# Optimization experiments

Measured on AMD Instinct MI355X. Metric: run time of the kernel, lower is better.

The kernel has to match this reference:

```python
import jax, jax.numpy as jnp
import numpy as np

D_MODEL = 1024
NHEAD = 16
DFF = 4096
EPS = 1e-5


def layer_norm(x, g, b, eps=EPS):
    mu = jnp.mean(x, axis=-1, keepdims=True)
    var = jnp.var(x, axis=-1, keepdims=True)
    return (x - mu) * jax.lax.rsqrt(var + eps) * g + b


def setup_inputs() -> dict:
    key = jax.random.key(0)
    ks = jax.random.split(key, 8)
    S, N, E = 1024, 8, D_MODEL
    s = 0.02
    return {
        "src": jax.random.normal(ks[0], (S, N, E), dtype=jnp.float32),
        "in_proj_w": jax.random.normal(ks[1], (3 * E, E), dtype=jnp.float32) * s,
        "in_proj_b": jnp.zeros((3 * E,), dtype=jnp.float32),
        "out_w": jax.random.normal(ks[2], (E, E), dtype=jnp.float32) * s,
        "out_b": jnp.zeros((E,), dtype=jnp.float32),
        "w1": jax.random.normal(ks[3], (DFF, E), dtype=jnp.float32) * s,
        "b1": jnp.zeros((DFF,), dtype=jnp.float32),
        "w2": jax.random.normal(ks[4], (E, DFF), dtype=jnp.float32) * s,
        "b2": jnp.zeros((E,), dtype=jnp.float32),
        "ln1_g": jnp.ones((E,), dtype=jnp.float32),
        "ln1_b": jnp.zeros((E,), dtype=jnp.float32),
        "ln2_g": jnp.ones((E,), dtype=jnp.float32),
        "ln2_b": jnp.zeros((E,), dtype=jnp.float32),
    }


def reference(src, in_proj_w, in_proj_b, out_w, out_b, w1, b1, w2, b2,
              ln1_g, ln1_b, ln2_g, ln2_b):
    S, N, E = src.shape
    H = NHEAD
    D = E // H
    scale = 1.0 / jnp.sqrt(jnp.asarray(D, src.dtype))

    # fused QKV projection (PyTorch in_proj): [S,N,3E]
    qkv = src @ in_proj_w.T + in_proj_b
    q, k, v = jnp.split(qkv, 3, axis=-1)
    # [S,N,E] -> [N,H,S,D]
    def to_heads(t):
        return t.reshape(S, N, H, D).transpose(1, 2, 0, 3)
    q, k, v = to_heads(q), to_heads(k), to_heads(v)

    # explicit QK^T / softmax / AV (need_weights=True path)
    scores = jnp.einsum('nhsd,nhtd->nhst', q * scale, k)  # [N,H,S,S]
    attn = jax.nn.softmax(scores, axis=-1)
    ctx = jnp.einsum('nhst,nhtd->nhsd', attn, v)          # [N,H,S,D]
    ctx = ctx.transpose(2, 0, 1, 3).reshape(S, N, E)
    attn_out = ctx @ out_w.T + out_b

    # avg over heads (PyTorch default average_attn_weights=True): [N,S,S]
    attn_weights = jnp.mean(attn, axis=1)

    # post-norm residual structure (norm_first=False), dropout=0 (eval)
    x = layer_norm(src + attn_out, ln1_g, ln1_b)
    ff = jax.nn.relu(x @ w1.T + b1) @ w2.T + b2
    x = layer_norm(x + ff, ln2_g, ln2_b)
    return x, attn_weights
```

## Files before the change

kernel.cpp:

```cpp
#include <hip/hip_runtime.h>

typedef __attribute__((ext_vector_type(4))) float f32x4;
typedef __attribute__((ext_vector_type(8))) short short8;
typedef __attribute__((ext_vector_type(4))) unsigned short u16x4;

#define MFMA(a,b,c) __builtin_amdgcn_mfma_f32_16x16x32_bf16(a,b,c,0,0,0)

__device__ __forceinline__ unsigned short f2bf(float x){
    union { float f; unsigned int u; } c; c.f = x;
    unsigned int u = c.u;
    unsigned int r = (u + 0x7fffu + ((u >> 16) & 1u)) >> 16;
    return (unsigned short)r;
}
__device__ __forceinline__ unsigned short tf2bf(float x){
    union { float f; unsigned int u; } c; c.f = x;
    return (unsigned short)(c.u >> 16);
}
__device__ __forceinline__ float bf2f(unsigned short h){
    union { unsigned int u; float f; } c; c.u = ((unsigned int)h) << 16;
    return c.f;
}

__device__ __forceinline__ void load16_lds(const unsigned short* g, unsigned short* l){
    __builtin_amdgcn_global_load_lds(
        (const __attribute__((address_space(1))) unsigned int*)g,
        (__attribute__((address_space(3))) unsigned int*)l, 16, 0, 0);
}

#define SWZ_IDX(row, col, stride) \
    ((row)*(stride) + (((((col) >> 3) ^ ((row) & 7)) << 3) | ((col) & 7)))

__global__ __launch_bounds__(256) void cast_f32_bf16(const float* __restrict__ in,
                                                     unsigned short* __restrict__ out, int n4){
    int i = blockIdx.x * 256 + threadIdx.x;
    if (i < n4){
        const float4* in4 = (const float4*)in;
        float4 v = in4[i];
        u16x4 o;
        o[0] = f2bf(v.x); o[1] = f2bf(v.y); o[2] = f2bf(v.z); o[3] = f2bf(v.w);
        ((u16x4*)out)[i] = o;
    }
}

template<int OUT_BF16, int RELU>
__global__ __launch_bounds__(512) void gemm256(const unsigned short* __restrict__ A,
                                               const unsigned short* __restrict__ W,
                                               const float* __restrict__ bias,
                                               void* __restrict__ Cout,
                                               int M, int N, int K)
{
    __shared__ unsigned short Asw[2][256*64];
    __shared__ unsigned short Bsw[2][256*64];
    const int tid  = threadIdx.x;
    const int wave = tid >> 6, lane = tid & 63;
    const int wr = wave >> 2, wc = wave & 3;
    const int lr = lane & 15, lg = lane >> 4;
    const int bm = blockIdx.x, bn = blockIdx.y;

    f32x4 acc[8][4] = {};

    const unsigned short* Ab = A + (size_t)bm*256*K;
    const unsigned short* Wb = W + (size_t)bn*256*K;

    auto stage = [&](int buf, int k0){
        #pragma unroll
        for (int i = 0; i < 4; ++i){
            int c = i*512 + tid;
            int row = c >> 3, sl = (c & 7) ^ (row & 7);
            load16_lds(Ab + (size_t)row*K + k0 + sl*8, &Asw[buf][0] + (size_t)c*8);
        }
        #pragma unroll
        for (int i = 0; i < 4; ++i){
            int c = i*512 + tid;
            int row = c >> 3, sl = (c & 7) ^ (row & 7);
            load16_lds(Wb + (size_t)row*K + k0 + sl*8, &Bsw[buf][0] + (size_t)c*8);
        }
    };

    stage(0, 0);
    const int NT = K >> 6;
    for (int t = 0; t < NT; ++t){
        const int cur = t & 1;
        if (t + 1 < NT){
            stage(cur ^ 1, (t+1) << 6);
            asm volatile("s_waitcnt vmcnt(8)" ::: "memory");
        } else {
            asm volatile("s_waitcnt vmcnt(0)" ::: "memory");
        }
        __builtin_amdgcn_s_barrier();
        asm volatile("" ::: "memory");
        const unsigned short* Al = &Asw[cur][0];
        const unsigned short* Bl = &Bsw[cur][0];
        #pragma unroll
        for (int kk = 0; kk < 2; ++kk){
            short8 af[8], bf[4];
            #pragma unroll
            for (int mi = 0; mi < 8; ++mi)
                af[mi] = *(const short8*)(Al + SWZ_IDX(wr*128 + mi*16 + lr, kk*32 + lg*8, 64));
            #pragma unroll
            for (int ni = 0; ni < 4; ++ni)
                bf[ni] = *(const short8*)(Bl + SWZ_IDX(wc*64 + ni*16 + lr, kk*32 + lg*8, 64));
            __builtin_amdgcn_s_setprio(1);
            #pragma unroll
            for (int mi = 0; mi < 8; ++mi)
                #pragma unroll
                for (int ni = 0; ni < 4; ++ni)
                    acc[mi][ni] = MFMA(af[mi], bf[ni], acc[mi][ni]);
            __builtin_amdgcn_s_setprio(0);
        }
        asm volatile("" ::: "memory");
        __builtin_amdgcn_s_barrier();
    }

    #pragma unroll
    for (int ni = 0; ni < 4; ++ni){
        int col = bn*256 + wc*64 + ni*16 + lr;
        float bv = bias ? bias[col] : 0.0f;
        #pragma unroll
        for (int mi = 0; mi < 8; ++mi){
            int row0 = bm*256 + wr*128 + mi*16 + lg*4;
            #pragma unroll
            for (int j = 0; j < 4; ++j){
                float v = acc[mi][ni][j] + bv;
                if (RELU) v = v > 0.0f ? v : 0.0f;
                if (OUT_BF16) ((unsigned short*)Cout)[(size_t)(row0+j)*N + col] = f2bf(v);
                else          ((float*)Cout)[(size_t)(row0+j)*N + col] = v;
            }
        }
    }
}

template<int OUT_BF16, int RELU>
__global__ __launch_bounds__(512) void gemm256x128(const unsigned short* __restrict__ A,
                                                   const unsigned short* __restrict__ W,
                                                   const float* __restrict__ bias,
                                                   void* __restrict__ Cout,
                                                   int M, int N, int K)
{
    __shared__ unsigned short Asw[2][256*64];
    __shared__ unsigned short Bsw[2][128*64];
    const int tid  = threadIdx.x;
    const int wave = tid >> 6, lane = tid & 63;
    const int wr = wave >> 1, wc = wave & 1;
    const int lr = lane & 15, lg = lane >> 4;
    const int bm = blockIdx.x, bn = blockIdx.y;

    f32x4 acc[4][4] = {};

    const unsigned short* Ab = A + (size_t)bm*256*K;
    const unsigned short* Wb = W + (size_t)bn*128*K;

    auto stage = [&](int buf, int k0){
        #pragma unroll
        for (int i = 0; i < 4; ++i){
            int c = i*512 + tid;
            int row = c >> 3, sl = (c & 7) ^ (row & 7);
            load16_lds(Ab + (size_t)row*K + k0 + sl*8, &Asw[buf][0] + (size_t)c*8);
        }
        #pragma unroll
        for (int i = 0; i < 2; ++i){
            int c = i*512 + tid;
            int row = c >> 3, sl = (c & 7) ^ (row & 7);
            load16_lds(Wb + (size_t)row*K + k0 + sl*8, &Bsw[buf][0] + (size_t)c*8);
        }
    };

    stage(0, 0);
    const int NT = K >> 6;
    for (int t = 0; t < NT; ++t){
        const int cur = t & 1;
        if (t + 1 < NT){
            stage(cur ^ 1, (t+1) << 6);
            asm volatile("s_waitcnt vmcnt(6)" ::: "memory");
        } else {
            asm volatile("s_waitcnt vmcnt(0)" ::: "memory");
        }
        __builtin_amdgcn_s_barrier();
        asm volatile("" ::: "memory");
        const unsigned short* Al = &Asw[cur][0];
        const unsigned short* Bl = &Bsw[cur][0];
        #pragma unroll
        for (int kk = 0; kk < 2; ++kk){
            short8 af[4], bf[4];
            #pragma unroll
            for (int mi = 0; mi < 4; ++mi)
                af[mi] = *(const short8*)(Al + SWZ_IDX(wr*64 + mi*16 + lr, kk*32 + lg*8, 64));
            #pragma unroll
            for (int ni = 0; ni < 4; ++ni)
                bf[ni] = *(const short8*)(Bl + SWZ_IDX(wc*64 + ni*16 + lr, kk*32 + lg*8, 64));
            __builtin_amdgcn_s_setprio(1);
            #pragma unroll
            for (int mi = 0; mi < 4; ++mi)
                #pragma unroll
                for (int ni = 0; ni < 4; ++ni)
                    acc[mi][ni] = MFMA(af[mi], bf[ni], acc[mi][ni]);
            __builtin_amdgcn_s_setprio(0);
        }
        asm volatile("" ::: "memory");
        __builtin_amdgcn_s_barrier();
    }

    #pragma unroll
    for (int ni = 0; ni < 4; ++ni){
        int col = bn*128 + wc*64 + ni*16 + lr;
        float bv = bias ? bias[col] : 0.0f;
        #pragma unroll
        for (int mi = 0; mi < 4; ++mi){
            int row0 = bm*256 + wr*64 + mi*16 + lg*4;
            #pragma unroll
            for (int j = 0; j < 4; ++j){
                float v = acc[mi][ni][j] + bv;
                if (RELU) v = v > 0.0f ? v : 0.0f;
                if (OUT_BF16) ((unsigned short*)Cout)[(size_t)(row0+j)*N + col] = f2bf(v);
                else          ((float*)Cout)[(size_t)(row0+j)*N + col] = v;
            }
        }
    }
}

__global__ __launch_bounds__(256) void transpose_v(const unsigned short* __restrict__ qkv,
                                                   unsigned short* __restrict__ vt)
{
    __shared__ unsigned short tile[64][80];
    const int tt = blockIdx.x, h = blockIdx.y, n = blockIdx.z;
    const int tid = threadIdx.x;
    #pragma unroll
    for (int i = 0; i < 2; ++i){
        int c = i*256 + tid;
        int row = c >> 3, cc = c & 7;
        short8 v = *(const short8*)(qkv + ((size_t)(tt*64+row)*8 + n)*3072 + 2048 + h*64 + cc*8);
        *(short8*)&tile[row][cc*8] = v;
    }
    __syncthreads();
    #pragma unroll
    for (int i = 0; i < 2; ++i){
        int c = i*256 + tid;
        int drow = c >> 3, cc = c & 7;
        short8 o;
        #pragma unroll
        for (int j = 0; j < 8; ++j) o[j] = tile[cc*8+j][drow];
        *(short8*)(vt + ((size_t)(n*16+h)*64 + drow)*1024 + tt*64 + cc*8) = o;
    }
}

template<int STORE_P8>
__global__ __launch_bounds__(256) void attn_fused(const unsigned short* __restrict__ qkv,
                                                  const unsigned short* __restrict__ vt,
                                                  float* __restrict__ stats,
                                                  unsigned short* __restrict__ ctx,
                                                  unsigned char* __restrict__ p8)
{
    __shared__ unsigned short qs[64*64];
    __shared__ unsigned short kt[2][64*64];
    __shared__ unsigned short vtile[2][64*64];
    __shared__ unsigned short pt[64*64];
    __shared__ float wl[4][64];
    __shared__ float rowinv[64];
    const int qb = blockIdx.x, h = blockIdx.y, n = blockIdx.z;
    const int tid = threadIdx.x;
    const int wave = tid >> 6, lane = tid & 63;
    const int lr = lane & 15, lg = lane >> 4;
    const int s0 = qb * 64;
    const float scale = 0.125f;
    const size_t plane = ((size_t)(n*16 + h)) << 20;

    #pragma unroll
    for (int i = 0; i < 2; ++i){
        int c = i*256 + tid;
        int row = c >> 3, cc = c & 7;
        *(short8*)(qs + SWZ_IDX(row, cc*8, 64)) =
            *(const short8*)(qkv + ((size_t)(s0+row)*8 + n)*3072 + h*64 + cc*8);
    }

    auto stageKV = [&](int buf, int tt){
        #pragma unroll
        for (int i = 0; i < 2; ++i){
            int c = wave*128 + i*64 + lane;
            int row = c >> 3, sl = (c & 7) ^ (row & 7);
            load16_lds(qkv + ((size_t)(tt*64+row)*8 + n)*3072 + 1024 + h*64 + sl*8,
                       &kt[buf][0] + (size_t)c*8);
            load16_lds(vt + ((size_t)(n*16+h)*64 + row)*1024 + tt*64 + sl*8,
                       &vtile[buf][0] + (size_t)c*8);
        }
    };

    stageKV(0, 0);
    __syncthreads();

    float lsum[4][4] = {};
    f32x4 av[4] = {};

    for (int tt = 0; tt < 16; ++tt){
        const int cur = tt & 1;
        if (tt + 1 < 16){
            stageKV(cur ^ 1, tt + 1);
            asm volatile("s_waitcnt vmcnt(4)" ::: "memory");
        } else {
            asm volatile("s_waitcnt vmcnt(0)" ::: "memory");
        }
        asm volatile("" ::: "memory");

        f32x4 acc[4] = {};
        #pragma unroll
        for (int kk = 0; kk < 2; ++kk){
            short8 b = *(const short8*)(&kt[cur][0] + SWZ_IDX(wave*16 + lr, kk*32 + lg*8, 64));
            __builtin_amdgcn_s_setprio(1);
            #pragma unroll
            for (int mi = 0; mi < 4; ++mi){
                short8 a = *(const short8*)(qs + SWZ_IDX(mi*16 + lr, kk*32 + lg*8, 64));
                acc[mi] = MFMA(a, b, acc[mi]);
            }
            __builtin_amdgcn_s_setprio(0);
        }
        unsigned short pv16[4][4];
        #pragma unroll
        for (int mi = 0; mi < 4; ++mi)
            #pragma unroll
            for (int j = 0; j < 4; ++j){
                float p = __expf(fminf(acc[mi][j] * scale, 80.0f));
                lsum[mi][j] += p;
                pv16[mi][j] = tf2bf(p);
            }

        __builtin_amdgcn_s_barrier();
        asm volatile("" ::: "memory");
        #pragma unroll
        for (int mi = 0; mi < 4; ++mi)
            #pragma unroll
            for (int j = 0; j < 4; ++j)
                pt[SWZ_IDX(mi*16 + lg*4 + j, wave*16 + lr, 64)] = pv16[mi][j];
        asm volatile("" ::: "memory");
        __builtin_amdgcn_s_barrier();

        #pragma unroll
        for (int kk = 0; kk < 2; ++kk){
            short8 b = *(const short8*)(&vtile[cur][0] + SWZ_IDX(wave*16 + lr, kk*32 + lg*8, 64));
            __builtin_amdgcn_s_setprio(1);
            #pragma unroll
            for (int mi = 0; mi < 4; ++mi){
                short8 a = *(const short8*)(pt + SWZ_IDX(mi*16 + lr, kk*32 + lg*8, 64));
                av[mi] = MFMA(a, b, av[mi]);
            }
            __builtin_amdgcn_s_setprio(0);
        }

        if (STORE_P8){
            #pragma unroll
            for (int i = 0; i < 2; ++i){
                int c = i*256 + tid;
                int prow = c >> 3, pcc = c & 7;
                short8 pv = *(const short8*)(pt + SWZ_IDX(prow, pcc*8, 64));
                unsigned int w0 = 0, w1 = 0;
                #pragma unroll
                for (int j = 0; j < 4; ++j){
                    unsigned int q = (unsigned int)fminf(bf2f((unsigned short)pv[j])*16.0f + 0.5f, 255.0f);
                    w0 |= q << (8*j);
                }
                #pragma unroll
                for (int j = 4; j < 8; ++j){
                    unsigned int q = (unsigned int)fminf(bf2f((unsigned short)pv[j])*16.0f + 0.5f, 255.0f);
                    w1 |= q << (8*(j-4));
                }
                uint2* dst = (uint2*)(p8 + plane + (size_t)(s0+prow)*1024 + tt*64 + pcc*8);
                *dst = make_uint2(w0, w1);
            }
        }
    }

    #pragma unroll
    for (int mi = 0; mi < 4; ++mi)
        #pragma unroll
        for (int j = 0; j < 4; ++j){
            float v = lsum[mi][j];
            v += __shfl_xor(v, 1);
            v += __shfl_xor(v, 2);
            v += __shfl_xor(v, 4);
            v += __shfl_xor(v, 8);
            if (lr == 0) wl[wave][mi*16 + lg*4 + j] = v;
        }
    __syncthreads();
    if (tid < 64){
        float l = wl[0][tid] + wl[1][tid] + wl[2][tid] + wl[3][tid];
        float inv = 1.0f / l;
        rowinv[tid] = inv;
        stats[((size_t)(n*16+h)*1024) + s0 + tid] = inv * 0.0625f;
    }
    __syncthreads();

    #pragma unroll
    for (int mi = 0; mi < 4; ++mi)
        #pragma unroll
        for (int j = 0; j < 4; ++j){
            int lrow = mi*16 + lg*4 + j;
            int srow = s0 + lrow;
            int d = wave*16 + lr;
            ctx[((size_t)srow*8 + n)*1024 + h*64 + d] = f2bf(av[mi][j] * rowinv[lrow]);
        }
}

__global__ __launch_bounds__(256) void attw_from_p8(const unsigned char* __restrict__ p8,
                                                    const float* __restrict__ stats,
                                                    float* __restrict__ attw)
{
    __shared__ float c[16];
    const int bid = blockIdx.x;
    const int n = bid >> 10, s = bid & 1023;
    const int tid = threadIdx.x;
    if (tid < 16) c[tid] = stats[(((size_t)(n*16 + tid)) << 10) + s] * (1.0f/16.0f);
    __syncthreads();
    float a0=0.f, a1=0.f, a2=0.f, a3=0.f;
    const unsigned char* base = p8 + ((size_t)n << 24) + ((size_t)s << 10) + tid*4;
    #pragma unroll
    for (int h = 0; h < 16; ++h){
        unsigned int v = *(const unsigned int*)(base + ((size_t)h << 20));
        float ch = c[h];
        a0 += (float)( v         & 255u) * ch;
        a1 += (float)((v >> 8 )  & 255u) * ch;
        a2 += (float)((v >> 16)  & 255u) * ch;
        a3 += (float)( v >> 24         ) * ch;
    }
    float4 o; o.x=a0; o.y=a1; o.z=a2; o.w=a3;
    *(float4*)(attw + ((size_t)bid << 10) + tid*4) = o;
}

__global__ __launch_bounds__(256) void attn_mean(const unsigned short* __restrict__ qkv,
                                                 const float* __restrict__ stats,
                                                 float* __restrict__ attw)
{
    __shared__ unsigned short qs[16*1024];
    __shared__ unsigned short kv[2][4][16*128];
    __shared__ float smL[16][16];
    const int qb = blockIdx.x, n = blockIdx.y;
    const int tid = threadIdx.x;
    const int wave = tid >> 6, lane = tid & 63;
    const int lr = lane & 15, lg = lane >> 4;
    const int s0 = qb * 16;
    const float scale = 0.125f;

    {
        int head = tid >> 4, row = tid & 15;
        smL[head][row] = stats[((size_t)(n*16+head)*1024) + s0 + row];
    }
    #pragma unroll
    for (int i = 0; i < 8; ++i){
        int c = i*256 + tid;
        int row = c >> 7, cc = c & 127;
        *(short8*)(qs + SWZ_IDX(row, cc*8, 1024)) =
            *(const short8*)(qkv + ((size_t)(s0+row)*8 + n)*3072 + cc*8);
    }

    unsigned short* kvw = &kv[0][wave][0];
    const int KVBUF = 4*16*128;

    auto stage = [&](int buf, int tt, int g){
        #pragma unroll
        for (int i = 0; i < 4; ++i){
            int c2 = i*64 + lane;
            int rw = c2 >> 4;
            int sd = c2 & 15;
            int sl = sd ^ (rw & 7);
            int trow = tt*64 + wave*16 + rw;
            load16_lds(qkv + ((size_t)trow*8 + n)*3072 + 1024 + g*128 + sl*8,
                       kvw + buf*KVBUF + i*512);
        }
    };

    __syncthreads();
    stage(0, 0, 0);

    float* obase = attw + (size_t)n*1024*1024;
    int r = 0;
    for (int tt = 0; tt < 16; ++tt){
        f32x4 racc = {0.0f, 0.0f, 0.0f, 0.0f};
        for (int g = 0; g < 8; ++g, ++r){
            int nr = r + 1;
            if (nr < 128) stage(nr & 1, nr >> 3, nr & 7);
            if (r < 127) asm volatile("s_waitcnt vmcnt(4)" ::: "memory");
            else         asm volatile("s_waitcnt vmcnt(0)" ::: "memory");
            const unsigned short* kb = kvw + (r & 1)*KVBUF;
            #pragma unroll
            for (int hh = 0; hh < 2; ++hh){
                f32x4 acc = {0.0f, 0.0f, 0.0f, 0.0f};
                #pragma unroll
                for (int kk = 0; kk < 2; ++kk){
                    short8 b = *(const short8*)(kb + SWZ_IDX(lr, hh*64 + kk*32 + lg*8, 128));
                    short8 a = *(const short8*)(qs + SWZ_IDX(lr, g*128 + hh*64 + kk*32 + lg*8, 1024));
                    acc = MFMA(a, b, acc);
                }
                #pragma unroll
                for (int j = 0; j < 4; ++j){
                    float sm = smL[g*2 + hh][lg*4 + j];
                    racc[j] += __expf(fminf(acc[j]*scale, 80.0f)) * sm;
                }
            }
        }
        #pragma unroll
        for (int j = 0; j < 4; ++j)
            obase[(size_t)(s0 + lg*4 + j)*1024 + tt*64 + wave*16 + lr] = racc[j];
    }
}

__global__ __launch_bounds__(256) void add_ln(const float* __restrict__ a,
                                              const float* __restrict__ b,
                                              const float* __restrict__ g,
                                              const float* __restrict__ be,
                                              float* __restrict__ out32,
                                              unsigned short* __restrict__ outbf)
{
    __shared__ float red[8];
    const int row = blockIdx.x;
    const int tid = threadIdx.x;
    const int wave = tid >> 6, lane = tid & 63;
    float4 va = ((const float4*)(a + (size_t)row*1024))[tid];
    float4 vb = ((const float4*)(b + (size_t)row*1024))[tid];
    float x0 = va.x + vb.x, x1 = va.y + vb.y, x2 = va.z + vb.z, x3 = va.w + vb.w;
    float s  = x0 + x1 + x2 + x3;
    float sq = x0*x0 + x1*x1 + x2*x2 + x3*x3;
    #pragma unroll
    for (int off = 1; off < 64; off <<= 1){
        s  += __shfl_xor(s,  off);
        sq += __shfl_xor(sq, off);
    }
    if (lane == 0){ red[wave] = s; red[4+wave] = sq; }
    __syncthreads();
    s  = red[0] + red[1] + red[2] + red[3];
    sq = red[4] + red[5] + red[6] + red[7];
    float mean = s * (1.0f/1024.0f);
    float var  = sq * (1.0f/1024.0f) - mean*mean;
    float rstd = rsqrtf(var + 1e-5f);
    int c = tid * 4;
    float4 vg = ((const float4*)(g  + c))[0];
    float4 vbeta = ((const float4*)(be + c))[0];
    float y0 = (x0-mean)*rstd*vg.x + vbeta.x;
    float y1 = (x1-mean)*rstd*vg.y + vbeta.y;
    float y2 = (x2-mean)*rstd*vg.z + vbeta.z;
    float y3 = (x3-mean)*rstd*vg.w + vbeta.w;
    float4 o; o.x=y0; o.y=y1; o.z=y2; o.w=y3;
    ((float4*)(out32 + (size_t)row*1024))[tid] = o;
    if (outbf){
        u16x4 ob; ob[0]=f2bf(y0); ob[1]=f2bf(y1); ob[2]=f2bf(y2); ob[3]=f2bf(y3);
        ((u16x4*)(outbf + (size_t)row*1024))[tid] = ob;
    }
}

extern "C" void kernel_launch(void* const* d_in, const int* in_sizes, int n_in,
                              void* d_out, int out_size, void* d_ws, size_t ws_size,
                              hipStream_t stream)
{
    (void)in_sizes; (void)n_in; (void)out_size;
    const float* src  = (const float*)d_in[0];
    const float* wqkv = (const float*)d_in[1];
    const float* bqkv = (const float*)d_in[2];
    const float* wout = (const float*)d_in[3];
    const float* bout = (const float*)d_in[4];
    const float* w1   = (const float*)d_in[5];
    const float* b1   = (const float*)d_in[6];
    const float* w2   = (const float*)d_in[7];
    const float* b2   = (const float*)d_in[8];
    const float* g1   = (const float*)d_in[9];
    const float* be1  = (const float*)d_in[10];
    const float* g2   = (const float*)d_in[11];
    const float* be2  = (const float*)d_in[12];

    char* ws = (char*)d_ws;
    const size_t MB = 1ull << 20;
    const bool fastp = (ws_size >= 250*MB);

    unsigned short *wqkv_bf, *wout_bf, *w1_bf, *w2_bf, *src_bf, *x1_bf;
    unsigned short *qkv_bf, *vt_bf, *ff1_bf, *ctx_bf;
    float *attn_out, *ff2_f32, *x1_f32, *stats;
    unsigned char* P8 = nullptr;

    if (fastp){
        wqkv_bf = (unsigned short*)(ws + 0*MB);
        wout_bf = (unsigned short*)(ws + 6*MB);
        w1_bf   = (unsigned short*)(ws + 8*MB);
        w2_bf   = (unsigned short*)(ws + 16*MB);
        src_bf  = (unsigned short*)(ws + 24*MB);
        x1_bf   = (unsigned short*)(ws + 24*MB);
        qkv_bf  = (unsigned short*)(ws + 40*MB);
        vt_bf   = (unsigned short*)(ws + 88*MB);
        ff1_bf  = (unsigned short*)(ws + 40*MB);
        ctx_bf  = (unsigned short*)(ws + 104*MB);
        stats   = (float*)(ws + 120*MB);
        P8      = (unsigned char*)(ws + 121*MB);
        attn_out= (float*)(ws + 121*MB);
        ff2_f32 = (float*)(ws + 121*MB);
        x1_f32  = (float*)(ws + 153*MB);
    } else {
        wqkv_bf = (unsigned short*)(ws + 0*MB);
        wout_bf = (unsigned short*)(ws + 6*MB);
        w1_bf   = (unsigned short*)(ws + 8*MB);
        w2_bf   = (unsigned short*)(ws + 16*MB);
        src_bf  = (unsigned short*)(ws + 24*MB);
        x1_bf   = (unsigned short*)(ws + 24*MB);
        qkv_bf  = (unsigned short*)(ws + 40*MB);
        vt_bf   = (unsigned short*)(ws + 88*MB);
        ff1_bf  = (unsigned short*)(ws + 40*MB);
        ctx_bf  = (unsigned short*)(ws + 104*MB);
        attn_out= (float*)(ws + 120*MB);
        ff2_f32 = (float*)(ws + 120*MB);
        x1_f32  = (float*)(ws + 152*MB);
        stats   = (float*)(ws + 184*MB);
    }

    float* x_out    = (float*)d_out;
    float* attw_out = (float*)d_out + (size_t)8192*1024;

    auto cast = [&](const float* in, unsigned short* out, int nelem){
        int n4 = nelem / 4;
        hipLaunchKernelGGL(cast_f32_bf16, dim3((n4 + 255)/256), dim3(256), 0, stream, in, out, n4);
    };
    cast(wqkv, wqkv_bf, 3072*1024);
    cast(wout, wout_bf, 1024*1024);
    cast(w1,   w1_bf,   4096*1024);
    cast(w2,   w2_bf,   1024*4096);
    cast(src,  src_bf,  8192*1024);

    hipLaunchKernelGGL((gemm256<1,0>), dim3(32,12), dim3(512), 0, stream,
                       src_bf, wqkv_bf, bqkv, (void*)qkv_bf, 8192, 3072, 1024);
    hipLaunchKernelGGL(transpose_v, dim3(16,16,8), dim3(256), 0, stream, qkv_bf, vt_bf);

    if (fastp){
        hipLaunchKernelGGL((attn_fused<1>), dim3(16,16,8), dim3(256), 0, stream,
                           qkv_bf, vt_bf, stats, ctx_bf, P8);
        hipLaunchKernelGGL(attw_from_p8, dim3(8192), dim3(256), 0, stream,
                           P8, stats, attw_out);
    } else {
        hipLaunchKernelGGL((attn_fused<0>), dim3(16,16,8), dim3(256), 0, stream,
                           qkv_bf, vt_bf, stats, ctx_bf, (unsigned char*)nullptr);
        hipLaunchKernelGGL(attn_mean, dim3(64,8), dim3(256), 0, stream,
                           qkv_bf, stats, attw_out);
    }

    hipLaunchKernelGGL((gemm256x128<0,0>), dim3(32,8), dim3(512), 0, stream,
                       ctx_bf, wout_bf, bout, (void*)attn_out, 8192, 1024, 1024);
    hipLaunchKernelGGL(add_ln, dim3(8192), dim3(256), 0, stream,
                       src, attn_out, g1, be1, x1_f32, x1_bf);
    hipLaunchKernelGGL((gemm256<1,1>), dim3(32,16), dim3(512), 0, stream,
                       x1_bf, w1_bf, b1, (void*)ff1_bf, 8192, 4096, 1024);
    hipLaunchKernelGGL((gemm256x128<0,0>), dim3(32,8), dim3(512), 0, stream,
                       ff1_bf, w2_bf, b2, (void*)ff2_f32, 8192, 1024, 4096);
    hipLaunchKernelGGL(add_ln, dim3(8192), dim3(256), 0, stream,
                       x1_f32, ff2_f32, g2, be2, x_out, nullptr);
}
```

Measured before the change: 521.8 us.

## Split GEMM main loop into quadrant phases interleaving next-tile staging

The 256x256 bf16 GEMM main loop is split into four phases, one per 128x128 output quadrant per wave group. Each phase issues one quarter of the next K-tile's global-to-LDS loads, then reads a subset of LDS fragments and runs its MFMA block. The goal is to spread memory traffic and LDS reads across the compute, instead of issuing all prefetches at once before a single wait. In exchange there are four barriers per K-step instead of two, and the fragment reuse pattern changes, which adds synchronisation overhead.

```diff
diff --git a/kernel.cpp b/kernel.cpp
--- a/kernel.cpp
+++ b/kernel.cpp
@@ -62,52 +62,102 @@
     const unsigned short* Ab = A + (size_t)bm*256*K;
     const unsigned short* Wb = W + (size_t)bn*256*K;
 
-    auto stage = [&](int buf, int k0){
-        #pragma unroll
-        for (int i = 0; i < 4; ++i){
+    auto stageHalf = [&](unsigned short* dstbase, const unsigned short* srcbase, int k0){
+        #pragma unroll
+        for (int i = 0; i < 2; ++i){
             int c = i*512 + tid;
             int row = c >> 3, sl = (c & 7) ^ (row & 7);
-            load16_lds(Ab + (size_t)row*K + k0 + sl*8, &Asw[buf][0] + (size_t)c*8);
-        }
-        #pragma unroll
-        for (int i = 0; i < 4; ++i){
-            int c = i*512 + tid;
-            int row = c >> 3, sl = (c & 7) ^ (row & 7);
-            load16_lds(Wb + (size_t)row*K + k0 + sl*8, &Bsw[buf][0] + (size_t)c*8);
+            load16_lds(srcbase + (size_t)row*K + k0 + sl*8, dstbase + (size_t)c*8);
         }
     };
 
-    stage(0, 0);
+    stageHalf(&Asw[0][0],    Ab,                 0);
+    stageHalf(&Asw[0][8192], Ab + (size_t)128*K, 0);
+    stageHalf(&Bsw[0][0],    Wb,                 0);
+    stageHalf(&Bsw[0][8192], Wb + (size_t)128*K, 0);
+
     const int NT = K >> 6;
     for (int t = 0; t < NT; ++t){
-        const int cur = t & 1;
-        if (t + 1 < NT){
-            stage(cur ^ 1, (t+1) << 6);
-            asm volatile("s_waitcnt vmcnt(8)" ::: "memory");
-        } else {
-            asm volatile("s_waitcnt vmcnt(0)" ::: "memory");
-        }
-        __builtin_amdgcn_s_barrier();
-        asm volatile("" ::: "memory");
+        const int cur = t & 1, nxt = cur ^ 1;
+        const bool pre = (t + 1 < NT);
+        const int k1 = (t + 1) << 6;
         const unsigned short* Al = &Asw[cur][0];
         const unsigned short* Bl = &Bsw[cur][0];
-        #pragma unroll
-        for (int kk = 0; kk < 2; ++kk){
-            short8 af[8], bf[4];
-            #pragma unroll
-            for (int mi = 0; mi < 8; ++mi)
-                af[mi] = *(const short8*)(Al + SWZ_IDX(wr*128 + mi*16 + lr, kk*32 + lg*8, 64));
-            #pragma unroll
-            for (int ni = 0; ni < 4; ++ni)
-                bf[ni] = *(const short8*)(Bl + SWZ_IDX(wc*64 + ni*16 + lr, kk*32 + lg*8, 64));
-            __builtin_amdgcn_s_setprio(1);
-            #pragma unroll
-            for (int mi = 0; mi < 8; ++mi)
-                #pragma unroll
-                for (int ni = 0; ni < 4; ++ni)
-                    acc[mi][ni] = MFMA(af[mi], bf[ni], acc[mi][ni]);
-            __builtin_amdgcn_s_setprio(0);
-        }
+        short8 af[4][2], bf[4][2];
+
+        if (pre) stageHalf(&Asw[nxt][0], Ab, k1);
+        if (pre) asm volatile("s_waitcnt vmcnt(2)" ::: "memory");
+        else     asm volatile("s_waitcnt vmcnt(0)" ::: "memory");
+        __builtin_amdgcn_s_barrier();
+        asm volatile("" ::: "memory");
+        #pragma unroll
+        for (int m = 0; m < 4; ++m)
+            #pragma unroll
+            for (int kk = 0; kk < 2; ++kk)
+                af[m][kk] = *(const short8*)(Al + SWZ_IDX(wr*128 + m*16 + lr, kk*32 + lg*8, 64));
+        #pragma unroll
+        for (int n2 = 0; n2 < 2; ++n2)
+            #pragma unroll
+            for (int kk = 0; kk < 2; ++kk)
+                bf[n2][kk] = *(const short8*)(Bl + SWZ_IDX(wc*64 + n2*16 + lr, kk*32 + lg*8, 64));
+        __builtin_amdgcn_s_setprio(1);
+        #pragma unroll
+        for (int kk = 0; kk < 2; ++kk)
+            #pragma unroll
+            for (int m = 0; m < 4; ++m)
+                #pragma unroll
+                for (int n2 = 0; n2 < 2; ++n2)
+                    acc[m][n2] = MFMA(af[m][kk], bf[n2][kk], acc[m][n2]);
+        __builtin_amdgcn_s_setprio(0);
+        asm volatile("" ::: "memory");
+        __builtin_amdgcn_s_barrier();
+
+        if (pre) stageHalf(&Asw[nxt][8192], Ab + (size_t)128*K, k1);
+        #pragma unroll
+        for (int n2 = 2; n2 < 4; ++n2)
+            #pragma unroll
+            for (int kk = 0; kk < 2; ++kk)
+                bf[n2][kk] = *(const short8*)(Bl + SWZ_IDX(wc*64 + n2*16 + lr, kk*32 + lg*8, 64));
+        __builtin_amdgcn_s_setprio(1);
+        #pragma unroll
+        for (int kk = 0; kk < 2; ++kk)
+            #pragma unroll
+            for (int m = 0; m < 4; ++m)
+                #pragma unroll
+                for (int n2 = 2; n2 < 4; ++n2)
+                    acc[m][n2] = MFMA(af[m][kk], bf[n2][kk], acc[m][n2]);
+        __builtin_amdgcn_s_setprio(0);
+        asm volatile("" ::: "memory");
+        __builtin_amdgcn_s_barrier();
+
+        if (pre) stageHalf(&Bsw[nxt][0], Wb, k1);
+        #pragma unroll
+        for (int m = 0; m < 4; ++m)
+            #pragma unroll
+            for (int kk = 0; kk < 2; ++kk)
+                af[m][kk] = *(const short8*)(Al + SWZ_IDX(wr*128 + 64 + m*16 + lr, kk*32 + lg*8, 64));
+        __builtin_amdgcn_s_setprio(1);
+        #pragma unroll
+        for (int kk = 0; kk < 2; ++kk)
+            #pragma unroll
+            for (int m = 0; m < 4; ++m)
+                #pragma unroll
+                for (int n2 = 0; n2 < 2; ++n2)
+                    acc[4 + m][n2] = MFMA(af[m][kk], bf[n2][kk], acc[4 + m][n2]);
+        __builtin_amdgcn_s_setprio(0);
+        asm volatile("" ::: "memory");
+        __builtin_amdgcn_s_barrier();
+
+        if (pre) stageHalf(&Bsw[nxt][8192], Wb + (size_t)128*K, k1);
+        __builtin_amdgcn_s_setprio(1);
+        #pragma unroll
+        for (int kk = 0; kk < 2; ++kk)
+            #pragma unroll
+            for (int m = 0; m < 4; ++m)
+                #pragma unroll
+                for (int n2 = 2; n2 < 4; ++n2)
+                    acc[4 + m][n2] = MFMA(af[m][kk], bf[n2][kk], acc[4 + m][n2]);
+        __builtin_amdgcn_s_setprio(0);
         asm volatile("" ::: "memory");
         __builtin_amdgcn_s_barrier();
     }
```

Result: slower. 533.0 us (+2.1%).
